# Kernel tuning notes

Measured on AMD Instinct MI355X. Metric: run time of the kernel, lower is better.

## Reference

```python
import jax, jax.numpy as jnp
import numpy as np

B, S, E, H = 8, 2048, 1024, 64  # batch, seq (== block_size), emb_size, head_size


def setup_inputs() -> dict:
    key = jax.random.key(0)
    ks = jax.random.split(key, 7)
    s = 1.0 / np.sqrt(E)  # ~ torch Linear default init scale
    return {
        "x": jax.random.normal(ks[0], (B, S, E), dtype=jnp.float32),
        "Wk": jax.random.uniform(ks[1], (H, E), jnp.float32, -s, s),
        "bk": jax.random.uniform(ks[2], (H,), jnp.float32, -s, s),
        "Wq": jax.random.uniform(ks[3], (H, E), jnp.float32, -s, s),
        "bq": jax.random.uniform(ks[4], (H,), jnp.float32, -s, s),
        "Wv": jax.random.uniform(ks[5], (H, E), jnp.float32, -s, s),
        "bv": jax.random.uniform(ks[6], (H,), jnp.float32, -s, s),
    }


def reference(x, Wk, bk, Wq, bq, Wv, bv):
    # Linear projections (torch Linear: y = x @ W.T + b)
    xk = jnp.einsum('bse,he->bsh', x, Wk) + bk  # [B,S,H]
    xq = jnp.einsum('bse,he->bsh', x, Wq) + bq
    xv = jnp.einsum('bse,he->bsh', x, Wv) + bv
    # raw scores q @ k^T  -> [B,S,S]
    wei = jnp.einsum('bqh,bkh->bqk', xq, xk)
    # causal mask (encoder=True branch in source; tril==0 -> -inf)
    causal = jnp.tril(jnp.ones((x.shape[1], x.shape[1]), dtype=bool))
    wei = jnp.where(causal, wei, -jnp.inf)
    # NOTE: source divides by head_size**(-0.5), i.e. MULTIPLIES by sqrt(head_size)
    scale = jnp.asarray(Wk.shape[0], jnp.float32) ** 0.5
    wei = jax.nn.softmax(wei * scale, axis=-1)
    return jnp.einsum('bqk,bkh->bqh', wei, xv)
```

## Files before the change

kernel.cpp:

```cpp
#include <hip/hip_runtime.h>

typedef _Float16 f16;
typedef _Float16 f16x8 __attribute__((ext_vector_type(8)));
typedef _Float16 f16x4 __attribute__((ext_vector_type(4)));
typedef __fp16 fp16x2 __attribute__((ext_vector_type(2)));
typedef float f32x4 __attribute__((ext_vector_type(4)));

#define MFMA16(a, b, c) __builtin_amdgcn_mfma_f32_16x16x32_f16(a, b, c, 0, 0, 0)

constexpr int Bn = 8, Sn = 2048, En = 1024, Hn = 64;
constexpr int Mn = Bn * Sn;
constexpr float QSCALE = 11.5415603f;
constexpr float THR = 11.5f;

__device__ __forceinline__ void gload_lds16(const void* g, void* lds) {
    __builtin_amdgcn_global_load_lds(
        (const __attribute__((address_space(1))) void*)g,
        (__attribute__((address_space(3))) void*)lds, 16, 0, 0);
}
__device__ __forceinline__ void wait_vm4() {
    asm volatile("s_waitcnt vmcnt(4)" ::: "memory");
    __builtin_amdgcn_sched_barrier(0);
}
__device__ __forceinline__ void wait_vm0() {
    asm volatile("s_waitcnt vmcnt(0)" ::: "memory");
    __builtin_amdgcn_sched_barrier(0);
}
__device__ __forceinline__ void barrier_raw() {
    __builtin_amdgcn_s_barrier();
    __builtin_amdgcn_sched_barrier(0);
}
__device__ __forceinline__ f16x8 cvt8(float4 lo, float4 hi) {
    union { f16x8 v; fp16x2 h[4]; } u;
    u.h[0] = __builtin_amdgcn_cvt_pkrtz(lo.x, lo.y);
    u.h[1] = __builtin_amdgcn_cvt_pkrtz(lo.z, lo.w);
    u.h[2] = __builtin_amdgcn_cvt_pkrtz(hi.x, hi.y);
    u.h[3] = __builtin_amdgcn_cvt_pkrtz(hi.z, hi.w);
    return u.v;
}


__global__ __launch_bounds__(256) void convw_kernel(
    const float* __restrict__ Wq, const float* __restrict__ Wk,
    const float* __restrict__ Wv, f16* __restrict__ Wc)
{
    const int h = blockIdx.x * 256 + threadIdx.x;
    const int kt = h / 1536;
    const int rem = h - kt * 1536;
    const int rr = rem >> 3;
    const int c = rem & 7;
    const int set = rr >> 6;
    const float* src = (set == 0 ? Wq : (set == 1 ? Wk : Wv))
                       + (size_t)(rr & 63) * En + kt * 64 + c * 8;
    float4 v0 = *reinterpret_cast<const float4*>(src);
    float4 v1 = *reinterpret_cast<const float4*>(src + 4);
    f16x8 o = cvt8(v0, v1);
    const int cs = c ^ (rr & 7);
    *reinterpret_cast<f16x8*>(Wc + (size_t)kt * 12288 + rr * 64 + cs * 8) = o;
}

__global__ __launch_bounds__(512) void proj_kernel(
    const float* __restrict__ x, const f16* __restrict__ Wc,
    const float* __restrict__ bq, const float* __restrict__ bk,
    const float* __restrict__ bv,
    f16* __restrict__ qws, f16* __restrict__ kws, f16* __restrict__ vtws)
{
    __shared__ __align__(16) char ldsb[2 * 32768];
    const int tid = threadIdx.x;
    const int w = tid >> 6, l = tid & 63;
    const int l15 = l & 15, lhi = l >> 4;
    const int rt = w & 1, nh = w >> 1;
    const int Mbase = blockIdx.x * 32;

    f32x4 acc[3];
#pragma unroll
    for (int i = 0; i < 3; ++i) acc[i] = (f32x4){0.f, 0.f, 0.f, 0.f};

    const int xr_s = w * 4 + (l >> 4);
    const int xc_s = (l & 15) ^ (xr_s & 7);

#define WSTAGE(buf, kb)                                                       \
    {                                                                         \
        const f16* wt_ = Wc + (size_t)(kb) * 12288;                           \
        _Pragma("unroll")                                                     \
        for (int r_ = 0; r_ < 3; ++r_)                                        \
            gload_lds16(wt_ + r_ * 4096 + w * 512 + l * 8,                    \
                        ldsb + (buf) * 32768 + r_ * 8192 + w * 1024);         \
    }

#define XSTAGE(buf, kb)                                                       \
    {                                                                         \
        const float* xs_ = x + (size_t)(Mbase + xr_s) * En + (kb) * 64        \
                           + xc_s * 4;                                        \
        gload_lds16(xs_, ldsb + (buf) * 32768 + 24576 + w * 1024);            \
    }

#define COMPUTE(buf)                                                          \
    {                                                                         \
        const int xrow_ = rt * 16 + l15;                                      \
        const char* xb_ = ldsb + (buf) * 32768 + 24576 + xrow_ * 256;         \
        f16x8 a_[2];                                                          \
        _Pragma("unroll")                                                     \
        for (int kc_ = 0; kc_ < 2; ++kc_) {                                   \
            const int c0_ = kc_ * 8 + lhi * 2;                                \
            float4 lo_ = *reinterpret_cast<const float4*>(                    \
                xb_ + ((c0_ ^ (l15 & 7)) * 16));                              \
            float4 hi_ = *reinterpret_cast<const float4*>(                    \
                xb_ + (((c0_ + 1) ^ (l15 & 7)) * 16));                        \
            a_[kc_] = cvt8(lo_, hi_);                                         \
        }                                                                     \
        _Pragma("unroll")                                                     \
        for (int i_ = 0; i_ < 3; ++i_) {                                      \
            const int row16_ = (nh * 3 + i_) * 16 + l15;                      \
            _Pragma("unroll")                                                 \
            for (int kc_ = 0; kc_ < 2; ++kc_) {                               \
                const int addr_ = (buf) * 32768 + row16_ * 128                \
                    + ((kc_ * 64 + lhi * 16) ^ ((l15 & 7) << 4));             \
                f16x8 b_ = *reinterpret_cast<const f16x8*>(ldsb + addr_);     \
                acc[i_] = MFMA16(a_[kc_], b_, acc[i_]);                       \
            }                                                                 \
        }                                                                     \
    }

    WSTAGE(0, 0);
    XSTAGE(0, 0);
#pragma unroll
    for (int i = 0; i < 16; ++i) {
        const int cur = i & 1;
        if (i < 15) {
            WSTAGE(cur ^ 1, i + 1);
            XSTAGE(cur ^ 1, i + 1);
            wait_vm4();
        } else {
            wait_vm0();
        }
        barrier_raw();
        COMPUTE(cur);
        barrier_raw();
    }
#undef WSTAGE
#undef XSTAGE
#undef COMPUTE

    const int batch = Mbase >> 11;
    const int r0 = Mbase + rt * 16 + lhi * 4;
#pragma unroll
    for (int i = 0; i < 3; ++i) {
        const int nt = nh * 3 + i;
        const int set = nt >> 2;
        const int h = (nt & 3) * 16 + l15;
        const float bias = (set == 0 ? bq : (set == 1 ? bk : bv))[h];
        if (set < 2) {
            f16* dst = (set == 0) ? qws : kws;
            const float scale = (set == 0) ? QSCALE : 1.0f;
            const int kc = h >> 5;
            const int lhk = (h >> 3) & 3;
            const int j = h & 7;
#pragma unroll
            for (int r = 0; r < 4; ++r) {
                const int s = (r0 + r) & (Sn - 1);
                const int t16 = s >> 4;
                const int l15k = s & 15;
                dst[(size_t)((batch * 128 + t16) * 2 + kc) * 512
                    + (lhk * 16 + l15k) * 8 + j] =
                    (f16)((acc[i][r] + bias) * scale);
            }
        } else {
            const int s0v = r0 & (Sn - 1);
            const int kt = s0v >> 5;
            const int spl = ((s0v & 12) << 1) + ((s0v & 16) ? 4 : 0);
            const int lhv = spl >> 3;
            const int j0 = spl & 7;
            const int ntv = h >> 4;
            const int l15v = h & 15;
            f16x4 hv = {(f16)(acc[i][0] + bias), (f16)(acc[i][1] + bias),
                        (f16)(acc[i][2] + bias), (f16)(acc[i][3] + bias)};
            *reinterpret_cast<f16x4*>(
                &vtws[(size_t)((batch * 64 + kt) * 4 + ntv) * 512
                      + (lhv * 16 + l15v) * 8 + j0]) = hv;
        }
    }
}

__global__ __launch_bounds__(256, 3) void attn_kernel(
    const f16* __restrict__ qws, const f16* __restrict__ kws,
    const f16* __restrict__ vtws, float* __restrict__ out,
    float* __restrict__ slots)
{
    const int tid = threadIdx.x;
    const int w = tid >> 6, l = tid & 63;
    const int l15 = l & 15, lhi = l >> 4;

    const int L = blockIdx.x * 4 + w;
    const int u = (int)(((unsigned)L * 997u) % 2304u);
    const int b = u / 288;
    const int t = u - b * 288;
    int k = 0;
#pragma unroll
    for (int gg = 1; gg < 8; ++gg)
        if (t >= 4 * gg * (gg + 1)) k = gg;
    const int rem = t - 4 * k * (k + 1);
    const int jq = rem / (k + 1);
    const int c = rem - jq * (k + 1);
    const int J = 8 * k + jq;

    const int qbase = J * 32;
    const int nkt = J + 1;
    const int ts = c * 8;
    const int te = (ts + 8 < nkt) ? ts + 8 : nkt;
    const bool hasDiag = (te == nkt);
    const int nfull = te - (hasDiag ? 1 : 0);

    f16x8 qf[2][2];
#pragma unroll
    for (int rs = 0; rs < 2; ++rs)
#pragma unroll
        for (int kc = 0; kc < 2; ++kc)
            qf[rs][kc] = *reinterpret_cast<const f16x8*>(
                &qws[(size_t)((b * 128 + J * 2 + rs) * 2 + kc) * 512 + l * 8]);

    f32x4 O[2][4];
#pragma unroll
    for (int rs = 0; rs < 2; ++rs)
#pragma unroll
        for (int nt = 0; nt < 4; ++nt) O[rs][nt] = (f32x4){0.f, 0.f, 0.f, 0.f};
    float m1[2] = {-1e30f, -1e30f}, l1[2] = {0.f, 0.f};

#define ATTN_ITER(KT, MASKED)                                                 \
    {                                                                         \
        f16x8 kf[2][2];                                                       \
        _Pragma("unroll") for (int nt = 0; nt < 2; ++nt)                      \
        _Pragma("unroll") for (int kc = 0; kc < 2; ++kc)                      \
            kf[nt][kc] = *reinterpret_cast<const f16x8*>(                     \
                &kws[(size_t)((b * 128 + (KT) * 2 + nt) * 2 + kc) * 512       \
                     + l * 8]);                                               \
        f32x4 Sv[2][2];                                                       \
        _Pragma("unroll") for (int rs = 0; rs < 2; ++rs)                      \
        _Pragma("unroll") for (int nt = 0; nt < 2; ++nt) {                    \
            f32x4 sa = (f32x4){0.f, 0.f, 0.f, 0.f};                           \
            sa = MFMA16(kf[nt][0], qf[rs][0], sa);                            \
            sa = MFMA16(kf[nt][1], qf[rs][1], sa);                            \
            Sv[rs][nt] = sa;                                                  \
        }                                                                     \
        float tv[2][2][4];                                                    \
        float mx[2];                                                          \
        _Pragma("unroll") for (int rs = 0; rs < 2; ++rs) {                    \
            _Pragma("unroll") for (int nt = 0; nt < 2; ++nt)                  \
            _Pragma("unroll") for (int r = 0; r < 4; ++r) {                   \
                float v = Sv[rs][nt][r];                                      \
                if (MASKED) {                                                 \
                    const int key_ = nt * 16 + lhi * 4 + r;                   \
                    const int qq_ = rs * 16 + l15;                            \
                    v = (key_ <= qq_) ? v : -1e30f;                           \
                }                                                             \
                tv[rs][nt][r] = v;                                            \
            }                                                                 \
            float a0 = fmaxf(fmaxf(tv[rs][0][0], tv[rs][0][1]),               \
                             fmaxf(tv[rs][0][2], tv[rs][0][3]));              \
            float a1 = fmaxf(fmaxf(tv[rs][1][0], tv[rs][1][1]),               \
                             fmaxf(tv[rs][1][2], tv[rs][1][3]));              \
            float m_ = fmaxf(a0, a1);                                         \
            m_ = fmaxf(m_, __shfl_xor(m_, 16));                               \
            m_ = fmaxf(m_, __shfl_xor(m_, 32));                               \
            mx[rs] = m_;                                                      \
        }                                                                     \
        const int need = (mx[0] > m1[0] + THR) || (mx[1] > m1[1] + THR);      \
        if (__any(need)) {                                                    \
            _Pragma("unroll") for (int rs = 0; rs < 2; ++rs) {                \
                const float mn = fmaxf(m1[rs], mx[rs]);                       \
                const float al = exp2f(m1[rs] - mn);                          \
                l1[rs] *= al;                                                 \
                _Pragma("unroll") for (int nt = 0; nt < 4; ++nt)              \
                _Pragma("unroll") for (int r = 0; r < 4; ++r)                 \
                    O[rs][nt][r] *= al;                                       \
                m1[rs] = mn;                                                  \
            }                                                                 \
        }                                                                     \
        f16x8 pa[2];                                                          \
        _Pragma("unroll") for (int rs = 0; rs < 2; ++rs) {                    \
            float p_[8];                                                      \
            float s_ = 0.f;                                                   \
            _Pragma("unroll") for (int nt = 0; nt < 2; ++nt)                  \
            _Pragma("unroll") for (int r = 0; r < 4; ++r) {                   \
                const float e_ = exp2f(tv[rs][nt][r] - m1[rs]);               \
                p_[nt * 4 + r] = e_;                                          \
                s_ += e_;                                                     \
            }                                                                 \
            s_ += __shfl_xor(s_, 16);                                         \
            s_ += __shfl_xor(s_, 32);                                         \
            l1[rs] += s_;                                                     \
            pa[rs] = (f16x8){(f16)p_[0], (f16)p_[1], (f16)p_[2], (f16)p_[3],  \
                             (f16)p_[4], (f16)p_[5], (f16)p_[6], (f16)p_[7]}; \
        }                                                                     \
        _Pragma("unroll") for (int nt = 0; nt < 4; ++nt) {                    \
            f16x8 vf = *reinterpret_cast<const f16x8*>(                       \
                &vtws[(size_t)((b * 64 + (KT)) * 4 + nt) * 512 + l * 8]);     \
            O[0][nt] = MFMA16(vf, pa[0], O[0][nt]);                           \
            O[1][nt] = MFMA16(vf, pa[1], O[1][nt]);                           \
        }                                                                     \
    }

    for (int kt = ts; kt < nfull; ++kt) ATTN_ITER(kt, false);
    if (hasDiag) ATTN_ITER(J, true);
#undef ATTN_ITER

    if (J < 8) {
#pragma unroll
        for (int rs = 0; rs < 2; ++rs) {
            const float inv = 1.0f / l1[rs];
            const size_t ro = ((size_t)b * Sn + qbase + rs * 16 + l15) * Hn;
#pragma unroll
            for (int nt = 0; nt < 4; ++nt) {
                float4 o = {O[rs][nt][0] * inv, O[rs][nt][1] * inv,
                            O[rs][nt][2] * inv, O[rs][nt][3] * inv};
                *reinterpret_cast<float4*>(&out[ro + nt * 16 + lhi * 4]) = o;
            }
        }
    } else {
        float* sl = slots + (size_t)(b * 280 + 4 * k * (k + 1) - 8
                                     + jq * (k + 1) + c) * 1088;
        f16* so = reinterpret_cast<f16*>(sl + 64);
#pragma unroll
        for (int rs = 0; rs < 2; ++rs) {
            const int row = rs * 16 + l15;
            const float inv = 1.0f / l1[rs];
            if (lhi == 0) { sl[row] = m1[rs]; sl[32 + row] = l1[rs]; }
#pragma unroll
            for (int nt = 0; nt < 4; ++nt) {
                f16x4 hv = {(f16)(O[rs][nt][0] * inv), (f16)(O[rs][nt][1] * inv),
                            (f16)(O[rs][nt][2] * inv), (f16)(O[rs][nt][3] * inv)};
                *reinterpret_cast<f16x4*>(
                    &so[row * 64 + nt * 16 + lhi * 4]) = hv;
            }
        }
    }
}

__global__ __launch_bounds__(256) void comb_kernel(
    const float* __restrict__ slots, float* __restrict__ out)
{
    const int id = blockIdx.x;
    const int b = id / 56, jj = id - b * 56;
    const int J = 8 + jj;
    const int k = J >> 3;
    const int nch = k + 1;
    const float* base = slots + (size_t)(b * 280 + 4 * k * (k + 1) - 8
                                         + (J - 8 * k) * (k + 1)) * 1088;
    const int tid = threadIdx.x;
    const int row = tid >> 3;
    const int h0 = (tid & 7) * 8;

    float mg = -1e30f;
    for (int cc = 0; cc < nch; ++cc)
        mg = fmaxf(mg, base[cc * 1088 + row]);
    float den = 0.f;
    float num[8] = {0.f, 0.f, 0.f, 0.f, 0.f, 0.f, 0.f, 0.f};
    for (int cc = 0; cc < nch; ++cc) {
        const float* sl = base + cc * 1088;
        const float wgt = sl[32 + row] * exp2f(sl[row] - mg);
        den += wgt;
        const f16* so = reinterpret_cast<const f16*>(sl + 64);
        f16x8 ov = *reinterpret_cast<const f16x8*>(&so[row * 64 + h0]);
#pragma unroll
        for (int i = 0; i < 8; ++i) num[i] += (float)ov[i] * wgt;
    }
    const float inv = 1.0f / den;
    const size_t ro = ((size_t)b * Sn + J * 32 + row) * Hn + h0;
    float4 o0 = {num[0] * inv, num[1] * inv, num[2] * inv, num[3] * inv};
    float4 o1 = {num[4] * inv, num[5] * inv, num[6] * inv, num[7] * inv};
    *reinterpret_cast<float4*>(&out[ro]) = o0;
    *reinterpret_cast<float4*>(&out[ro + 4]) = o1;
}

extern "C" void kernel_launch(void* const* d_in, const int* in_sizes, int n_in,
                              void* d_out, int out_size, void* d_ws, size_t ws_size,
                              hipStream_t stream) {
    const float* x  = (const float*)d_in[0];
    const float* Wk = (const float*)d_in[1];
    const float* bk = (const float*)d_in[2];
    const float* Wq = (const float*)d_in[3];
    const float* bq = (const float*)d_in[4];
    const float* Wv = (const float*)d_in[5];
    const float* bv = (const float*)d_in[6];

    f16* qws  = (f16*)d_ws;
    f16* kws  = qws + (size_t)Mn * Hn;
    f16* vtws = kws + (size_t)Mn * Hn;
    f16* Wc   = vtws + (size_t)Mn * Hn;
    float* slots = (float*)(Wc + 196608);

    convw_kernel<<<96, 256, 0, stream>>>(Wq, Wk, Wv, Wc);
    proj_kernel<<<512, 512, 0, stream>>>(x, Wc, bq, bk, bv, qws, kws, vtws);
    attn_kernel<<<576, 256, 0, stream>>>(qws, kws, vtws, (float*)d_out, slots);
    comb_kernel<<<448, 256, 0, stream>>>(slots, (float*)d_out);
}
```

Baseline: 53.28 us.

## Split projection workgroups across output halves to double grid and shrink LDS

The projection kernel now launches 1024 workgroups of 256 threads, each computing half of the 192 QKV output columns for a 32-row tile, instead of 512 workgroups of 512 threads computing all columns. LDS per block falls from 64KB to 40KB and launch bounds ask for 4 blocks per CU, aiming for better occupancy and more parallelism across CUs. The cost is that each x tile is loaded twice (once per half), which adds global read traffic on the largest input. The staging loops and vmcnt wait are adjusted to match the new per-wave load counts.

```diff
diff --git a/kernel.cpp b/kernel.cpp
--- a/kernel.cpp
+++ b/kernel.cpp
@@ -18,8 +18,8 @@
         (const __attribute__((address_space(1))) void*)g,
         (__attribute__((address_space(3))) void*)lds, 16, 0, 0);
 }
-__device__ __forceinline__ void wait_vm4() {
-    asm volatile("s_waitcnt vmcnt(4)" ::: "memory");
+__device__ __forceinline__ void wait_vm5() {
+    asm volatile("s_waitcnt vmcnt(5)" ::: "memory");
     __builtin_amdgcn_sched_barrier(0);
 }
 __device__ __forceinline__ void wait_vm0() {
@@ -59,46 +59,52 @@
     *reinterpret_cast<f16x8*>(Wc + (size_t)kt * 12288 + rr * 64 + cs * 8) = o;
 }
 
-__global__ __launch_bounds__(512) void proj_kernel(
+__global__ __launch_bounds__(256, 4) void proj_kernel(
     const float* __restrict__ x, const f16* __restrict__ Wc,
     const float* __restrict__ bq, const float* __restrict__ bk,
     const float* __restrict__ bv,
     f16* __restrict__ qws, f16* __restrict__ kws, f16* __restrict__ vtws)
 {
-    __shared__ __align__(16) char ldsb[2 * 32768];
+    __shared__ __align__(16) char ldsb[2 * 20480];
     const int tid = threadIdx.x;
     const int w = tid >> 6, l = tid & 63;
     const int l15 = l & 15, lhi = l >> 4;
-    const int rt = w & 1, nh = w >> 1;
-    const int Mbase = blockIdx.x * 32;
+    const int rt = w & 1, npair = w >> 1;
+    const int wg = blockIdx.x;
+    const int mp = wg >> 1, nhalf = wg & 1;
+    const int Mbase = mp * 32;
 
     f32x4 acc[3];
 #pragma unroll
     for (int i = 0; i < 3; ++i) acc[i] = (f32x4){0.f, 0.f, 0.f, 0.f};
-
-    const int xr_s = w * 4 + (l >> 4);
-    const int xc_s = (l & 15) ^ (xr_s & 7);
 
 #define WSTAGE(buf, kb)                                                       \
     {                                                                         \
-        const f16* wt_ = Wc + (size_t)(kb) * 12288;                           \
+        const f16* wt_ = Wc + (size_t)(kb) * 12288 + nhalf * 6144;            \
         _Pragma("unroll")                                                     \
-        for (int r_ = 0; r_ < 3; ++r_)                                        \
-            gload_lds16(wt_ + r_ * 4096 + w * 512 + l * 8,                    \
-                        ldsb + (buf) * 32768 + r_ * 8192 + w * 1024);         \
+        for (int r_ = 0; r_ < 3; ++r_) {                                      \
+            const int g_ = w * 3 + r_;                                        \
+            gload_lds16(wt_ + g_ * 512 + l * 8,                               \
+                        ldsb + (buf) * 20480 + g_ * 1024);                    \
+        }                                                                     \
     }
 
 #define XSTAGE(buf, kb)                                                       \
     {                                                                         \
-        const float* xs_ = x + (size_t)(Mbase + xr_s) * En + (kb) * 64        \
-                           + xc_s * 4;                                        \
-        gload_lds16(xs_, ldsb + (buf) * 32768 + 24576 + w * 1024);            \
+        _Pragma("unroll")                                                     \
+        for (int e_ = 0; e_ < 2; ++e_) {                                      \
+            const int gx_ = w * 2 + e_;                                       \
+            const int r_ = gx_ * 4 + (l >> 4);                                \
+            const float* xs_ = x + (size_t)(Mbase + r_) * En + (kb) * 64      \
+                               + (((l & 15) ^ (r_ & 7)) * 4);                 \
+            gload_lds16(xs_, ldsb + (buf) * 20480 + 12288 + gx_ * 1024);      \
+        }                                                                     \
     }
 
 #define COMPUTE(buf)                                                          \
     {                                                                         \
         const int xrow_ = rt * 16 + l15;                                      \
-        const char* xb_ = ldsb + (buf) * 32768 + 24576 + xrow_ * 256;         \
+        const char* xb_ = ldsb + (buf) * 20480 + 12288 + xrow_ * 256;         \
         f16x8 a_[2];                                                          \
         _Pragma("unroll")                                                     \
         for (int kc_ = 0; kc_ < 2; ++kc_) {                                   \
@@ -111,10 +117,10 @@
         }                                                                     \
         _Pragma("unroll")                                                     \
         for (int i_ = 0; i_ < 3; ++i_) {                                      \
-            const int row16_ = (nh * 3 + i_) * 16 + l15;                      \
+            const int row16_ = (npair * 3 + i_) * 16 + l15;                   \
             _Pragma("unroll")                                                 \
             for (int kc_ = 0; kc_ < 2; ++kc_) {                               \
-                const int addr_ = (buf) * 32768 + row16_ * 128                \
+                const int addr_ = (buf) * 20480 + row16_ * 128                \
                     + ((kc_ * 64 + lhi * 16) ^ ((l15 & 7) << 4));             \
                 f16x8 b_ = *reinterpret_cast<const f16x8*>(ldsb + addr_);     \
                 acc[i_] = MFMA16(a_[kc_], b_, acc[i_]);                       \
@@ -130,7 +136,7 @@
         if (i < 15) {
             WSTAGE(cur ^ 1, i + 1);
             XSTAGE(cur ^ 1, i + 1);
-            wait_vm4();
+            wait_vm5();
         } else {
             wait_vm0();
         }
@@ -146,7 +152,7 @@
     const int r0 = Mbase + rt * 16 + lhi * 4;
 #pragma unroll
     for (int i = 0; i < 3; ++i) {
-        const int nt = nh * 3 + i;
+        const int nt = nhalf * 6 + npair * 3 + i;
         const int set = nt >> 2;
         const int h = (nt & 3) * 16 + l15;
         const float bias = (set == 0 ? bq : (set == 1 ? bk : bv))[h];
@@ -390,7 +396,7 @@
     float* slots = (float*)(Wc + 196608);
 
     convw_kernel<<<96, 256, 0, stream>>>(Wq, Wk, Wv, Wc);
-    proj_kernel<<<512, 512, 0, stream>>>(x, Wc, bq, bk, bv, qws, kws, vtws);
+    proj_kernel<<<1024, 256, 0, stream>>>(x, Wc, bq, bk, bv, qws, kws, vtws);
     attn_kernel<<<576, 256, 0, stream>>>(qws, kws, vtws, (float*)d_out, slots);
     comb_kernel<<<448, 256, 0, stream>>>(slots, (float*)d_out);
 }
```

New measurement: 61.80 us. +16.0%, slower.
